# Kernel optimization log

Measured on AMD Instinct MI355X. Metric: run time of the kernel, lower is better.

The kernel has to match this reference:

```python
import jax, jax.numpy as jnp
import numpy as np

_INV_SQRT2 = np.float32(0.7071067811865476)


def _dwt_last(u):
    """Single-level Haar DWT along the last axis (pywt 'haar' convention).
    cA[i] = (u[2i]+u[2i+1])/sqrt(2), cD[i] = (u[2i]-u[2i+1])/sqrt(2)."""
    e = u[..., 0::2]
    o = u[..., 1::2]
    return (e + o) * _INV_SQRT2, (e - o) * _INV_SQRT2


def _dwt2(x):
    """Single-level 2D Haar DWT over the last two axes, matching pywt.dwt2.
    Returns (cA, cH, cV, cD) = ('aa', 'da', 'ad', 'dd') where the first
    letter is the filter applied along axis -2 and the second along axis -1."""
    a1, d1 = _dwt_last(x)                      # filter along axis -1
    a1t, d1t = a1.swapaxes(-1, -2), d1.swapaxes(-1, -2)
    aa, da = _dwt_last(a1t)                    # filter along axis -2
    ad, dd = _dwt_last(d1t)
    return (aa.swapaxes(-1, -2), da.swapaxes(-1, -2),
            ad.swapaxes(-1, -2), dd.swapaxes(-1, -2))


def setup_inputs() -> dict:
    key = jax.random.key(0)
    B, C, H, W = 32, 3, 512, 512
    x = jax.random.normal(key, (B, C, H, W), dtype=jnp.float32)
    return {"x": x}


def reference(x):
    # pywt.wavedec2(x, 'haar', level=2) -> [cA2, (cH2,cV2,cD2), (cH1,cV1,cD1)]
    a1, h1, v1, d1 = _dwt2(x)    # level 1: [B,C,H/2,W/2]
    a2, h2, v2, d2 = _dwt2(a1)   # level 2: [B,C,H/4,W/4]
    return (a2, h2, v2, d2, h1, v1, d1)
```

## Files before the change

kernel.cpp:

```cpp
#include <hip/hip_runtime.h>


#define KINV 0.7071067811865476f

typedef float v4f __attribute__((ext_vector_type(4)));
typedef float v2f __attribute__((ext_vector_type(2)));

#define QUADS(b, aa, da, ad, dd)                                          \
    do {                                                                  \
        _Pragma("unroll")                                                 \
        for (int i = 0; i < 2; ++i) {                                     \
            const float q00 = b[2*i].x,   q01 = b[2*i].y;                 \
            const float q02 = b[2*i].z,   q03 = b[2*i].w;                 \
            const float q10 = b[2*i+1].x, q11 = b[2*i+1].y;               \
            const float q12 = b[2*i+1].z, q13 = b[2*i+1].w;               \
            {                                                             \
                const float sA = (q00 + q01) * KINV;                      \
                const float sB = (q10 + q11) * KINV;                      \
                const float dA = (q00 - q01) * KINV;                      \
                const float dB = (q10 - q11) * KINV;                      \
                aa[i][0] = (sA + sB) * KINV;                              \
                da[i][0] = (sA - sB) * KINV;                              \
                ad[i][0] = (dA + dB) * KINV;                              \
                dd[i][0] = (dA - dB) * KINV;                              \
            }                                                             \
            {                                                             \
                const float sA = (q02 + q03) * KINV;                      \
                const float sB = (q12 + q13) * KINV;                      \
                const float dA = (q02 - q03) * KINV;                      \
                const float dB = (q12 - q13) * KINV;                      \
                aa[i][1] = (sA + sB) * KINV;                              \
                da[i][1] = (sA - sB) * KINV;                              \
                ad[i][1] = (dA + dB) * KINV;                              \
                dd[i][1] = (dA - dB) * KINV;                              \
            }                                                             \
        }                                                                 \
    } while (0)

__global__ __launch_bounds__(256, 4) void haar2_fused_kernel(
    const float* __restrict__ x, float* __restrict__ out, int nimg)
{
    const int tid = blockIdx.x * blockDim.x + threadIdx.x;
    const int cx  = tid & 63;
    const int r2  = (tid >> 6) & 127;
    const int img = tid >> 13;

    const int row0 = r2 * 4;
    const int col0 = cx * 8;

    const size_t n2 = (size_t)nimg * 128 * 128;
    const size_t n1 = (size_t)nimg * 256 * 256;
    float* a2o = out;
    float* h2o = out + n2;
    float* v2o = out + 2 * n2;
    float* d2o = out + 3 * n2;
    float* h1o = out + 4 * n2;
    float* v1o = h1o + n1;
    float* d1o = h1o + 2 * n1;

    const size_t in_base = (size_t)img * (512 * 512) + (size_t)row0 * 512 + col0;
    v4f bA[4], bB[4];
    #pragma unroll
    for (int k = 0; k < 4; ++k) {
        bA[k] = *reinterpret_cast<const v4f*>(x + in_base + (size_t)k * 512);
        bB[k] = *reinterpret_cast<const v4f*>(x + in_base + (size_t)k * 512 + 4);
    }

    float aaL[2][2], daL[2][2], adL[2][2], ddL[2][2];
    QUADS(bA, aaL, daL, adL, ddL);
    float aaR[2][2], daR[2][2], adR[2][2], ddR[2][2];
    QUADS(bB, aaR, daR, adR, ddR);

    const size_t img1 = (size_t)img * 256 * 256;
    #pragma unroll
    for (int i = 0; i < 2; ++i) {
        const size_t off = img1 + (size_t)(2 * r2 + i) * 256 + 4 * cx;
        __builtin_nontemporal_store((v4f){daL[i][0], daL[i][1], daR[i][0], daR[i][1]},
                                    reinterpret_cast<v4f*>(h1o + off));
        __builtin_nontemporal_store((v4f){adL[i][0], adL[i][1], adR[i][0], adR[i][1]},
                                    reinterpret_cast<v4f*>(v1o + off));
        __builtin_nontemporal_store((v4f){ddL[i][0], ddL[i][1], ddR[i][0], ddR[i][1]},
                                    reinterpret_cast<v4f*>(d1o + off));
    }

    const float s0L = (aaL[0][0] + aaL[0][1]) * KINV;
    const float d0L = (aaL[0][0] - aaL[0][1]) * KINV;
    const float s1L = (aaL[1][0] + aaL[1][1]) * KINV;
    const float d1L = (aaL[1][0] - aaL[1][1]) * KINV;
    const float s0R = (aaR[0][0] + aaR[0][1]) * KINV;
    const float d0R = (aaR[0][0] - aaR[0][1]) * KINV;
    const float s1R = (aaR[1][0] + aaR[1][1]) * KINV;
    const float d1R = (aaR[1][0] - aaR[1][1]) * KINV;

    const size_t off2 = (size_t)img * 128 * 128 + (size_t)r2 * 128 + 2 * cx;
    __builtin_nontemporal_store((v2f){(s0L + s1L) * KINV, (s0R + s1R) * KINV},
                                reinterpret_cast<v2f*>(a2o + off2));
    __builtin_nontemporal_store((v2f){(s0L - s1L) * KINV, (s0R - s1R) * KINV},
                                reinterpret_cast<v2f*>(h2o + off2));
    __builtin_nontemporal_store((v2f){(d0L + d1L) * KINV, (d0R + d1R) * KINV},
                                reinterpret_cast<v2f*>(v2o + off2));
    __builtin_nontemporal_store((v2f){(d0L - d1L) * KINV, (d0R - d1R) * KINV},
                                reinterpret_cast<v2f*>(d2o + off2));
}

extern "C" void kernel_launch(void* const* d_in, const int* in_sizes, int n_in,
                              void* d_out, int out_size, void* d_ws, size_t ws_size,
                              hipStream_t stream) {
    const float* x = (const float*)d_in[0];
    float* out = (float*)d_out;
    const int nimg = in_sizes[0] / (512 * 512);
    const int total_threads = nimg * 128 * 64;
    const int block = 256;
    const int grid = total_threads / block;
    haar2_fused_kernel<<<grid, block, 0, stream>>>(x, out, nimg);
}
```

Baseline: 175.5 us.

## Stage input stripes into LDS via direct global-to-LDS loads

Each block now loads a contiguous 16-row stripe of an image into shared memory using global_load_lds DMA (16-byte per lane, fully coalesced), waits on vmcnt, then each wave reads its 4 rows from LDS to compute both Haar levels. This replaces strided per-thread vector loads from global memory with contiguous streaming loads, aiming for better DRAM access efficiency. It adds 32KB of LDS per block and a serial load-then-compute phase with no overlap between them. The grid is now one block per stripe per image.

```diff
diff --git a/kernel.cpp b/kernel.cpp
--- a/kernel.cpp
+++ b/kernel.cpp
@@ -6,47 +6,20 @@
 typedef float v4f __attribute__((ext_vector_type(4)));
 typedef float v2f __attribute__((ext_vector_type(2)));
 
-#define QUADS(b, aa, da, ad, dd)                                          \
-    do {                                                                  \
-        _Pragma("unroll")                                                 \
-        for (int i = 0; i < 2; ++i) {                                     \
-            const float q00 = b[2*i].x,   q01 = b[2*i].y;                 \
-            const float q02 = b[2*i].z,   q03 = b[2*i].w;                 \
-            const float q10 = b[2*i+1].x, q11 = b[2*i+1].y;               \
-            const float q12 = b[2*i+1].z, q13 = b[2*i+1].w;               \
-            {                                                             \
-                const float sA = (q00 + q01) * KINV;                      \
-                const float sB = (q10 + q11) * KINV;                      \
-                const float dA = (q00 - q01) * KINV;                      \
-                const float dB = (q10 - q11) * KINV;                      \
-                aa[i][0] = (sA + sB) * KINV;                              \
-                da[i][0] = (sA - sB) * KINV;                              \
-                ad[i][0] = (dA + dB) * KINV;                              \
-                dd[i][0] = (dA - dB) * KINV;                              \
-            }                                                             \
-            {                                                             \
-                const float sA = (q02 + q03) * KINV;                      \
-                const float sB = (q12 + q13) * KINV;                      \
-                const float dA = (q02 - q03) * KINV;                      \
-                const float dB = (q12 - q13) * KINV;                      \
-                aa[i][1] = (sA + sB) * KINV;                              \
-                da[i][1] = (sA - sB) * KINV;                              \
-                ad[i][1] = (dA + dB) * KINV;                              \
-                dd[i][1] = (dA - dB) * KINV;                              \
-            }                                                             \
-        }                                                                 \
-    } while (0)
+#define STRIPE_ROWS 16
+#define LDS_FLOATS (STRIPE_ROWS * 512)
 
-__global__ __launch_bounds__(256, 4) void haar2_fused_kernel(
+__global__ __launch_bounds__(256) void haar2_fused_kernel(
     const float* __restrict__ x, float* __restrict__ out, int nimg)
 {
-    const int tid = blockIdx.x * blockDim.x + threadIdx.x;
-    const int cx  = tid & 63;
-    const int r2  = (tid >> 6) & 127;
-    const int img = tid >> 13;
+    __shared__ float lds[LDS_FLOATS];
 
-    const int row0 = r2 * 4;
-    const int col0 = cx * 8;
+    const int tid  = threadIdx.x;
+    const int lane = tid & 63;
+    const int w    = tid >> 6;
+    const int blk    = blockIdx.x;
+    const int stripe = blk & 31;
+    const int img    = blk >> 5;
 
     const size_t n2 = (size_t)nimg * 128 * 128;
     const size_t n1 = (size_t)nimg * 256 * 256;
@@ -58,23 +31,65 @@
     float* v1o = h1o + n1;
     float* d1o = h1o + 2 * n1;
 
-    const size_t in_base = (size_t)img * (512 * 512) + (size_t)row0 * 512 + col0;
-    v4f bA[4], bB[4];
+    const size_t stripe_base =
+        (size_t)img * (512 * 512) + (size_t)stripe * (STRIPE_ROWS * 512);
+
+    {
+        const float* gsrc = x + stripe_base + (size_t)(w * 2048) + (size_t)(lane * 4);
+        float* ldst = &lds[w * 2048];
+        #pragma unroll
+        for (int j = 0; j < 8; ++j) {
+            __builtin_amdgcn_global_load_lds(
+                (const __attribute__((address_space(1))) void*)(gsrc + j * 256),
+                (__attribute__((address_space(3))) void*)(ldst + j * 256),
+                16, 0, 0);
+        }
+    }
+    asm volatile("s_waitcnt vmcnt(0)" ::: "memory");
+    __builtin_amdgcn_sched_barrier(0);
+
+    const int cx = lane;
+    v4f L[4], R[4];
     #pragma unroll
-    for (int k = 0; k < 4; ++k) {
-        bA[k] = *reinterpret_cast<const v4f*>(x + in_base + (size_t)k * 512);
-        bB[k] = *reinterpret_cast<const v4f*>(x + in_base + (size_t)k * 512 + 4);
+    for (int r = 0; r < 4; ++r) {
+        const float* p = &lds[(w * 4 + r) * 512 + cx * 8];
+        L[r] = *reinterpret_cast<const v4f*>(p);
+        R[r] = *reinterpret_cast<const v4f*>(p + 4);
     }
 
     float aaL[2][2], daL[2][2], adL[2][2], ddL[2][2];
-    QUADS(bA, aaL, daL, adL, ddL);
     float aaR[2][2], daR[2][2], adR[2][2], ddR[2][2];
-    QUADS(bB, aaR, daR, adR, ddR);
+    #pragma unroll
+    for (int i = 0; i < 2; ++i) {
+        {
+            const v4f top = L[2 * i], bot = L[2 * i + 1];
+            const float sA0 = (top.x + top.y) * KINV, dA0 = (top.x - top.y) * KINV;
+            const float sB0 = (bot.x + bot.y) * KINV, dB0 = (bot.x - bot.y) * KINV;
+            aaL[i][0] = (sA0 + sB0) * KINV; daL[i][0] = (sA0 - sB0) * KINV;
+            adL[i][0] = (dA0 + dB0) * KINV; ddL[i][0] = (dA0 - dB0) * KINV;
+            const float sA1 = (top.z + top.w) * KINV, dA1 = (top.z - top.w) * KINV;
+            const float sB1 = (bot.z + bot.w) * KINV, dB1 = (bot.z - bot.w) * KINV;
+            aaL[i][1] = (sA1 + sB1) * KINV; daL[i][1] = (sA1 - sB1) * KINV;
+            adL[i][1] = (dA1 + dB1) * KINV; ddL[i][1] = (dA1 - dB1) * KINV;
+        }
+        {
+            const v4f top = R[2 * i], bot = R[2 * i + 1];
+            const float sA0 = (top.x + top.y) * KINV, dA0 = (top.x - top.y) * KINV;
+            const float sB0 = (bot.x + bot.y) * KINV, dB0 = (bot.x - bot.y) * KINV;
+            aaR[i][0] = (sA0 + sB0) * KINV; daR[i][0] = (sA0 - sB0) * KINV;
+            adR[i][0] = (dA0 + dB0) * KINV; ddR[i][0] = (dA0 - dB0) * KINV;
+            const float sA1 = (top.z + top.w) * KINV, dA1 = (top.z - top.w) * KINV;
+            const float sB1 = (bot.z + bot.w) * KINV, dB1 = (bot.z - bot.w) * KINV;
+            aaR[i][1] = (sA1 + sB1) * KINV; daR[i][1] = (sA1 - sB1) * KINV;
+            adR[i][1] = (dA1 + dB1) * KINV; ddR[i][1] = (dA1 - dB1) * KINV;
+        }
+    }
 
     const size_t img1 = (size_t)img * 256 * 256;
+    const int l1row = stripe * 8 + w * 2;
     #pragma unroll
     for (int i = 0; i < 2; ++i) {
-        const size_t off = img1 + (size_t)(2 * r2 + i) * 256 + 4 * cx;
+        const size_t off = img1 + (size_t)(l1row + i) * 256 + (size_t)cx * 4;
         __builtin_nontemporal_store((v4f){daL[i][0], daL[i][1], daR[i][0], daR[i][1]},
                                     reinterpret_cast<v4f*>(h1o + off));
         __builtin_nontemporal_store((v4f){adL[i][0], adL[i][1], adR[i][0], adR[i][1]},
@@ -92,7 +107,8 @@
     const float s1R = (aaR[1][0] + aaR[1][1]) * KINV;
     const float d1R = (aaR[1][0] - aaR[1][1]) * KINV;
 
-    const size_t off2 = (size_t)img * 128 * 128 + (size_t)r2 * 128 + 2 * cx;
+    const size_t off2 = (size_t)img * (128 * 128)
+                      + (size_t)(stripe * 4 + w) * 128 + (size_t)cx * 2;
     __builtin_nontemporal_store((v2f){(s0L + s1L) * KINV, (s0R + s1R) * KINV},
                                 reinterpret_cast<v2f*>(a2o + off2));
     __builtin_nontemporal_store((v2f){(s0L - s1L) * KINV, (s0R - s1R) * KINV},
@@ -109,8 +125,7 @@
     const float* x = (const float*)d_in[0];
     float* out = (float*)d_out;
     const int nimg = in_sizes[0] / (512 * 512);
-    const int total_threads = nimg * 128 * 64;
+    const int grid = nimg * 32;
     const int block = 256;
-    const int grid = total_threads / block;
     haar2_fused_kernel<<<grid, block, 0, stream>>>(x, out, nimg);
 }
```

Measured after the change: 176.5 us. About the same (+0.6%).
